# Performance work log

Measured on AMD Instinct MI355X. Metric: run time of the kernel, lower is better.

## Reference

```python
import jax, jax.numpy as jnp
import numpy as np

TOKENS = 64
IN_F = 8192
OUT_F = 8192
CODESZ = 8
CB_SIZE = 256


def fwht(x):
    """Sylvester fast Walsh-Hadamard transform along last dim. x: (B, n), n power of 2."""
    b, n = x.shape
    h = 1
    while h < n:
        x = x.reshape(b, n // (2 * h), 2, h)
        x = jnp.concatenate([x[:, :, :1] + x[:, :, 1:], x[:, :, :1] - x[:, :, 1:]], axis=2)
        x = x.reshape(b, n)
        h *= 2
    return x


def setup_inputs() -> dict:
    key = jax.random.key(0)
    k0, k1, k2, k3, k4, k5 = jax.random.split(key, 6)
    x = jax.random.normal(k0, (TOKENS, IN_F), jnp.float32)
    # SU/SV are random sign vectors in QuIP
    SU = jnp.sign(jax.random.normal(k1, (IN_F,), jnp.float32))
    SV = jnp.sign(jax.random.normal(k2, (OUT_F,), jnp.float32))
    grid = jax.random.normal(k3, (CB_SIZE, CODESZ), jnp.float32)  # codebook entries
    Wscale = jnp.ones((1,), jnp.float32)
    bias = jax.random.normal(k4, (OUT_F,), jnp.float32) * 0.01
    Qidxs = jax.random.randint(k5, (OUT_F, IN_F // CODESZ), 0, CB_SIZE, jnp.int32)
    return {"x": x, "SU": SU, "SV": SV, "grid": grid, "Wscale": Wscale, "bias": bias, "Qidxs": Qidxs}


def reference(x, SU, SV, grid, Wscale, bias, Qidxs):
    # 1) input sign scale
    xs = x * SU
    # 2) matmul_hadUt with folded wscale: x @ H^T / sqrt(n_in) * wscale (H symmetric Sylvester)
    inv_sqrt_in = 1.0 / jnp.sqrt(jnp.asarray(IN_F, x.dtype))
    xh = fwht(xs) * (inv_sqrt_in * Wscale[0])
    # 3) codebook dequant + matmul: W_hat[o, i] from codebook lookup, out = xh @ W_hat^T
    W_hat = grid[Qidxs].reshape(OUT_F, IN_F)  # (out, in) dequantized weight
    y = xh @ W_hat.T  # (tokens, out)
    # 4) matmul_hadU on the output side, truncate to out_features (no-op here: q_out == out)
    inv_sqrt_out = 1.0 / jnp.sqrt(jnp.asarray(OUT_F, x.dtype))
    yh = fwht(y) * inv_sqrt_out
    yh = yh[..., :OUT_F]
    # 5) output sign scale + bias
    return yh * SV + bias
```

## Files before the change

### kernel.cpp

```cpp
#include <hip/hip_runtime.h>
#include <hip/hip_bf16.h>

#define TOKENS 64
#define IN_F 8192
#define OUT_F 8192
#define CB 256

typedef _Float16 half8 __attribute__((ext_vector_type(8)));
typedef float f32x4 __attribute__((ext_vector_type(4)));

__global__ __launch_bounds__(256) void k_fwht_in(const float* __restrict__ x,
                                                 const float* __restrict__ SU,
                                                 const float* __restrict__ Wscale,
                                                 _Float16* __restrict__ xh_frag)
{
    __shared__ float buf[256 * 33];
    __shared__ _Float16 xrowP[256 * 40];
    const int t    = threadIdx.x;
    const int lane = t & 63;
    const int w    = t >> 6;
    const int row  = blockIdx.x;

    float v[32];
    const float* xr = x + row * IN_F;
#pragma unroll
    for (int rh = 0; rh < 8; ++rh) {
        int base = (rh << 10) | (t << 2);
        float4 xv = *(const float4*)(xr + base);
        float4 sv = *(const float4*)(SU + base);
        v[rh * 4 + 0] = xv.x * sv.x;
        v[rh * 4 + 1] = xv.y * sv.y;
        v[rh * 4 + 2] = xv.z * sv.z;
        v[rh * 4 + 3] = xv.w * sv.w;
    }
#pragma unroll
    for (int h = 1; h < 32; h <<= 1) {
#pragma unroll
        for (int r = 0; r < 32; ++r) {
            if ((r & h) == 0) {
                float a = v[r], b = v[r + h];
                v[r] = a + b;
                v[r + h] = a - b;
            }
        }
    }
#pragma unroll
    for (int m = 1; m < 64; m <<= 1) {
        bool upper = (lane & m) != 0;
#pragma unroll
        for (int r = 0; r < 32; ++r) {
            float p = __shfl_xor(v[r], m, 64);
            v[r] = upper ? (p - v[r]) : (v[r] + p);
        }
    }
#pragma unroll
    for (int r = 0; r < 32; ++r) buf[t * 33 + r] = v[r];
    __syncthreads();
    {
        float s1 = (w & 1) ? -1.f : 1.f;
        float s2 = (w & 2) ? -1.f : 1.f;
        float s3 = s1 * s2;
#pragma unroll
        for (int r = 0; r < 32; ++r) {
            float a0 = buf[(0 * 64 + lane) * 33 + r];
            float a1 = buf[(1 * 64 + lane) * 33 + r];
            float a2 = buf[(2 * 64 + lane) * 33 + r];
            float a3 = buf[(3 * 64 + lane) * 33 + r];
            v[r] = a0 + s1 * a1 + s2 * a2 + s3 * a3;
        }
    }
    const float scale = 0.011048543456039806f * Wscale[0];
#pragma unroll
    for (int r = 0; r < 32; ++r) {
        int c = ((r >> 2) << 10) | (t << 2) | (r & 3);
        int idx = (c & 31) + (c >> 5) * 40;
        xrowP[idx] = (_Float16)(v[r] * scale);
    }
    __syncthreads();
    {
        const int mt  = row >> 4;
        const int l15 = row & 15;
        _Float16* base = xh_frag + ((size_t)(t * 4 + mt) * 64 + l15) * 8;
#pragma unroll
        for (int g = 0; g < 4; ++g) {
            half8 val = *(const half8*)&xrowP[t * 40 + g * 8];
            *(half8*)(base + g * 16 * 8) = val;
        }
    }
}

#define SQWW 17
__global__ __launch_bounds__(256, 2) void k_qgemm(const _Float16* __restrict__ xh_frag,
                                                  const int* __restrict__ Qidxs,
                                                  const float* __restrict__ grid,
                                                  float* __restrict__ y_part)
{
    __shared__ __align__(16) _Float16 glds[CB * 8];
    __shared__ __align__(16) unsigned int uni[4 * 64 * SQWW];
    float* red = (float*)uni;

    const int tid  = threadIdx.x;
    const int lane = tid & 63;
    const int w    = tid >> 6;
    const int col  = lane & 15;
    const int quad = lane >> 4;
    const int g    = blockIdx.x >> 2;
    const int p    = blockIdx.x & 3;
    const int n0   = g * 64;

    unsigned int* sqw = uni + w * (64 * SQWW);

    {
        const int* qbase = Qidxs + (size_t)n0 * 1024 + p * 256 + w * 64 + col * 4;
#pragma unroll
        for (int i = 0; i < 16; ++i) {
            int r = i * 4 + quad;
            int4 vv = *(const int4*)(qbase + (size_t)r * 1024);
            unsigned int pk = (unsigned int)(vv.x & 255) |
                              ((unsigned int)(vv.y & 255) << 8) |
                              ((unsigned int)(vv.z & 255) << 16) |
                              ((unsigned int)(vv.w & 255) << 24);
            sqw[r * SQWW + col] = pk;
        }
    }
    {
#pragma unroll
        for (int e = 0; e < 4; ++e) {
            int entry = lane + 64 * e;
            float4 g0 = *((const float4*)grid + entry * 2);
            float4 g1 = *((const float4*)grid + entry * 2 + 1);
            half8 hv;
            hv[0] = (_Float16)g0.x; hv[1] = (_Float16)g0.y;
            hv[2] = (_Float16)g0.z; hv[3] = (_Float16)g0.w;
            hv[4] = (_Float16)g1.x; hv[5] = (_Float16)g1.y;
            hv[6] = (_Float16)g1.z; hv[7] = (_Float16)g1.w;
            *(half8*)&glds[entry * 8] = hv;
        }
    }
    __asm__ volatile("s_waitcnt lgkmcnt(0)" ::: "memory");
    __builtin_amdgcn_sched_barrier(0);

    const int shq = quad * 8;

#define QWREAD(dst, s_)                                              \
    {                                                                \
        dst[0] = sqw[(0 * 16 + col) * SQWW + (s_)];                  \
        dst[1] = sqw[(1 * 16 + col) * SQWW + (s_)];                  \
        dst[2] = sqw[(2 * 16 + col) * SQWW + (s_)];                  \
        dst[3] = sqw[(3 * 16 + col) * SQWW + (s_)];                  \
    }

    const _Float16* abase = xh_frag + ((size_t)(p * 64 + w * 16) * 4 * 64 + lane) * 8;

    f32x4 acc[4][4] = {};

    unsigned int qw_c[4], qw_n[4];
    QWREAD(qw_c, 0);
    QWREAD(qw_n, 1);
    half8 b_c[4];
#pragma unroll
    for (int nt = 0; nt < 4; ++nt) {
        unsigned int q = (qw_c[nt] >> shq) & 255u;
        b_c[nt] = *(const half8*)&glds[q * 8];
    }
    half8 a_c[4], a_n[4];
#pragma unroll
    for (int mt = 0; mt < 4; ++mt) {
        a_c[mt] = *(const half8*)(abase + (size_t)(0 * 4 + mt) * 512);
        a_n[mt] = *(const half8*)(abase + (size_t)(1 * 4 + mt) * 512);
    }

#pragma unroll 4
    for (int s = 0; s < 16; ++s) {
        const int s2q = (s + 2 < 16 ? s + 2 : 15);
        unsigned int qw_nn[4];
        QWREAD(qw_nn, s2q);
        half8 b_n[4], a_nn[4];
#pragma unroll
        for (int nt = 0; nt < 4; ++nt) {
            unsigned int q = (qw_n[nt] >> shq) & 255u;
            b_n[nt] = *(const half8*)&glds[q * 8];
        }
#pragma unroll
        for (int mt = 0; mt < 4; ++mt)
            a_nn[mt] = *(const half8*)(abase + (size_t)(s2q * 4 + mt) * 512);
#pragma unroll
        for (int nt = 0; nt < 4; ++nt)
#pragma unroll
            for (int mt = 0; mt < 4; ++mt)
                acc[nt][mt] = __builtin_amdgcn_mfma_f32_16x16x32_f16(
                    a_c[mt], b_c[nt], acc[nt][mt], 0, 0, 0);
#pragma unroll
        for (int nt = 0; nt < 4; ++nt) { b_c[nt] = b_n[nt]; qw_n[nt] = qw_nn[nt]; }
#pragma unroll
        for (int mt = 0; mt < 4; ++mt) { a_c[mt] = a_n[mt]; a_n[mt] = a_nn[mt]; }
    }

    float* redw = red + w * (64 * SQWW);
    float* yp = y_part + (size_t)p * TOKENS * OUT_F;
#pragma unroll
    for (int nt = 0; nt < 4; ++nt) {
#pragma unroll
        for (int mt = 0; mt < 4; ++mt)
#pragma unroll
            for (int i = 0; i < 4; ++i) {
                int r = mt * 16 + quad * 4 + i;
                redw[r * SQWW + col] = acc[nt][mt][i];
            }
        __syncthreads();
#pragma unroll
        for (int j = 0; j < 4; ++j) {
            int idx = j * 256 + tid;
            int rr = idx >> 4;
            int cc = idx & 15;
            float s = (red[(0 * 64 + rr) * SQWW + cc] + red[(1 * 64 + rr) * SQWW + cc])
                    + (red[(2 * 64 + rr) * SQWW + cc] + red[(3 * 64 + rr) * SQWW + cc]);
            yp[(size_t)rr * OUT_F + n0 + nt * 16 + cc] = s;
        }
        __syncthreads();
    }
#undef QWREAD
}

__global__ __launch_bounds__(256) void k_fwht_out(const float* __restrict__ y_part,
                                                  const float* __restrict__ SV,
                                                  const float* __restrict__ bias,
                                                  float* __restrict__ out)
{
    __shared__ float buf[256 * 33];
    const int t    = threadIdx.x;
    const int lane = t & 63;
    const int w    = t >> 6;
    const int row  = blockIdx.x;

    const float* y0 = y_part + (size_t)row * OUT_F;
    const size_t ps = (size_t)TOKENS * OUT_F;

    float v[32];
#pragma unroll
    for (int rh = 0; rh < 8; ++rh) {
        int base = (rh << 10) | (t << 2);
        float4 a = *(const float4*)(y0 + base);
        float4 b = *(const float4*)(y0 + ps + base);
        float4 c = *(const float4*)(y0 + 2 * ps + base);
        float4 d = *(const float4*)(y0 + 3 * ps + base);
        v[rh * 4 + 0] = (a.x + b.x) + (c.x + d.x);
        v[rh * 4 + 1] = (a.y + b.y) + (c.y + d.y);
        v[rh * 4 + 2] = (a.z + b.z) + (c.z + d.z);
        v[rh * 4 + 3] = (a.w + b.w) + (c.w + d.w);
    }
#pragma unroll
    for (int h = 1; h < 32; h <<= 1) {
#pragma unroll
        for (int r = 0; r < 32; ++r) {
            if ((r & h) == 0) {
                float a = v[r], b = v[r + h];
                v[r] = a + b;
                v[r + h] = a - b;
            }
        }
    }
#pragma unroll
    for (int m = 1; m < 64; m <<= 1) {
        bool upper = (lane & m) != 0;
#pragma unroll
        for (int r = 0; r < 32; ++r) {
            float p = __shfl_xor(v[r], m, 64);
            v[r] = upper ? (p - v[r]) : (v[r] + p);
        }
    }
#pragma unroll
    for (int r = 0; r < 32; ++r) buf[t * 33 + r] = v[r];
    __syncthreads();
    {
        float s1 = (w & 1) ? -1.f : 1.f;
        float s2 = (w & 2) ? -1.f : 1.f;
        float s3 = s1 * s2;
#pragma unroll
        for (int r = 0; r < 32; ++r) {
            float a0 = buf[(0 * 64 + lane) * 33 + r];
            float a1 = buf[(1 * 64 + lane) * 33 + r];
            float a2 = buf[(2 * 64 + lane) * 33 + r];
            float a3 = buf[(3 * 64 + lane) * 33 + r];
            v[r] = a0 + s1 * a1 + s2 * a2 + s3 * a3;
        }
    }
    const float scale = 0.011048543456039806f;
    float* oo = out + (size_t)row * OUT_F;
#pragma unroll
    for (int rh = 0; rh < 8; ++rh) {
        int base = (rh << 10) | (t << 2);
        float4 sv = *(const float4*)(SV + base);
        float4 bv = *(const float4*)(bias + base);
        float4 o;
        o.x = v[rh * 4 + 0] * scale * sv.x + bv.x;
        o.y = v[rh * 4 + 1] * scale * sv.y + bv.y;
        o.z = v[rh * 4 + 2] * scale * sv.z + bv.z;
        o.w = v[rh * 4 + 3] * scale * sv.w + bv.w;
        *(float4*)(oo + base) = o;
    }
}

extern "C" void kernel_launch(void* const* d_in, const int* in_sizes, int n_in,
                              void* d_out, int out_size, void* d_ws, size_t ws_size,
                              hipStream_t stream) {
    const float* x      = (const float*)d_in[0];
    const float* SU     = (const float*)d_in[1];
    const float* SV     = (const float*)d_in[2];
    const float* grid   = (const float*)d_in[3];
    const float* Wscale = (const float*)d_in[4];
    const float* bias   = (const float*)d_in[5];
    const int*   Qidxs  = (const int*)d_in[6];
    float* out = (float*)d_out;

    _Float16* xh_frag = (_Float16*)d_ws;
    float*    y_part  = (float*)((char*)d_ws + ((size_t)1 << 20));

    k_fwht_in<<<TOKENS, 256, 0, stream>>>(x, SU, Wscale, xh_frag);
    k_qgemm<<<512, 256, 0, stream>>>(xh_frag, Qidxs, grid, y_part);
    k_fwht_out<<<TOKENS, 256, 0, stream>>>(y_part, SV, bias, out);
}
```

Baseline: 110.8 us.

## Store split-K partials in fp16, fully unroll loop, raise MFMA priority

```diff
diff --git a/kernel.cpp b/kernel.cpp
--- a/kernel.cpp
+++ b/kernel.cpp
@@ -7,6 +7,7 @@
 #define CB 256
 
 typedef _Float16 half8 __attribute__((ext_vector_type(8)));
+typedef _Float16 half4v __attribute__((ext_vector_type(4)));
 typedef float f32x4 __attribute__((ext_vector_type(4)));
 
 __global__ __launch_bounds__(256) void k_fwht_in(const float* __restrict__ x,
@@ -93,7 +94,7 @@
 __global__ __launch_bounds__(256, 2) void k_qgemm(const _Float16* __restrict__ xh_frag,
                                                   const int* __restrict__ Qidxs,
                                                   const float* __restrict__ grid,
-                                                  float* __restrict__ y_part)
+                                                  _Float16* __restrict__ y_part)
 {
     __shared__ __align__(16) _Float16 glds[CB * 8];
     __shared__ __align__(16) unsigned int uni[4 * 64 * SQWW];
@@ -170,7 +171,7 @@
         a_n[mt] = *(const half8*)(abase + (size_t)(1 * 4 + mt) * 512);
     }
 
-#pragma unroll 4
+#pragma unroll
     for (int s = 0; s < 16; ++s) {
         const int s2q = (s + 2 < 16 ? s + 2 : 15);
         unsigned int qw_nn[4];
@@ -184,12 +185,14 @@
 #pragma unroll
         for (int mt = 0; mt < 4; ++mt)
             a_nn[mt] = *(const half8*)(abase + (size_t)(s2q * 4 + mt) * 512);
+        __builtin_amdgcn_s_setprio(1);
 #pragma unroll
         for (int nt = 0; nt < 4; ++nt)
 #pragma unroll
             for (int mt = 0; mt < 4; ++mt)
                 acc[nt][mt] = __builtin_amdgcn_mfma_f32_16x16x32_f16(
                     a_c[mt], b_c[nt], acc[nt][mt], 0, 0, 0);
+        __builtin_amdgcn_s_setprio(0);
 #pragma unroll
         for (int nt = 0; nt < 4; ++nt) { b_c[nt] = b_n[nt]; qw_n[nt] = qw_nn[nt]; }
 #pragma unroll
@@ -197,7 +200,7 @@
     }
 
     float* redw = red + w * (64 * SQWW);
-    float* yp = y_part + (size_t)p * TOKENS * OUT_F;
+    _Float16* yp = y_part + (size_t)p * TOKENS * OUT_F;
 #pragma unroll
     for (int nt = 0; nt < 4; ++nt) {
 #pragma unroll
@@ -215,14 +218,14 @@
             int cc = idx & 15;
             float s = (red[(0 * 64 + rr) * SQWW + cc] + red[(1 * 64 + rr) * SQWW + cc])
                     + (red[(2 * 64 + rr) * SQWW + cc] + red[(3 * 64 + rr) * SQWW + cc]);
-            yp[(size_t)rr * OUT_F + n0 + nt * 16 + cc] = s;
+            yp[(size_t)rr * OUT_F + n0 + nt * 16 + cc] = (_Float16)s;
         }
         __syncthreads();
     }
 #undef QWREAD
 }
 
-__global__ __launch_bounds__(256) void k_fwht_out(const float* __restrict__ y_part,
+__global__ __launch_bounds__(256) void k_fwht_out(const _Float16* __restrict__ y_part,
                                                   const float* __restrict__ SV,
                                                   const float* __restrict__ bias,
                                                   float* __restrict__ out)
@@ -233,21 +236,20 @@
     const int w    = t >> 6;
     const int row  = blockIdx.x;
 
-    const float* y0 = y_part + (size_t)row * OUT_F;
+    const _Float16* y0 = y_part + (size_t)row * OUT_F;
     const size_t ps = (size_t)TOKENS * OUT_F;
 
     float v[32];
 #pragma unroll
     for (int rh = 0; rh < 8; ++rh) {
         int base = (rh << 10) | (t << 2);
-        float4 a = *(const float4*)(y0 + base);
-        float4 b = *(const float4*)(y0 + ps + base);
-        float4 c = *(const float4*)(y0 + 2 * ps + base);
-        float4 d = *(const float4*)(y0 + 3 * ps + base);
-        v[rh * 4 + 0] = (a.x + b.x) + (c.x + d.x);
-        v[rh * 4 + 1] = (a.y + b.y) + (c.y + d.y);
-        v[rh * 4 + 2] = (a.z + b.z) + (c.z + d.z);
-        v[rh * 4 + 3] = (a.w + b.w) + (c.w + d.w);
+        half4v a = *(const half4v*)(y0 + base);
+        half4v b = *(const half4v*)(y0 + ps + base);
+        half4v c = *(const half4v*)(y0 + 2 * ps + base);
+        half4v d = *(const half4v*)(y0 + 3 * ps + base);
+#pragma unroll
+        for (int q = 0; q < 4; ++q)
+            v[rh * 4 + q] = ((float)a[q] + (float)b[q]) + ((float)c[q] + (float)d[q]);
     }
 #pragma unroll
     for (int h = 1; h < 32; h <<= 1) {
@@ -314,7 +316,7 @@
     float* out = (float*)d_out;
 
     _Float16* xh_frag = (_Float16*)d_ws;
-    float*    y_part  = (float*)((char*)d_ws + ((size_t)1 << 20));
+    _Float16* y_part  = (_Float16*)((char*)d_ws + ((size_t)1 << 20));
 
     k_fwht_in<<<TOKENS, 256, 0, stream>>>(x, SU, Wscale, xh_frag);
     k_qgemm<<<512, 256, 0, stream>>>(xh_frag, Qidxs, grid, y_part);
```

Result: no change. 110.6 us (-0.1%).
